# Kernel tuning notes

Measured on AMD Instinct MI355X. Metric: run time of the kernel, lower is better.

Reference implementation:

```python
import jax, jax.numpy as jnp
import numpy as np

B, T, D, H, L = 32, 512, 1024, 1024, 2


def setup_inputs() -> dict:
    key = jax.random.key(0)
    ks = jax.random.split(key, 7)
    s_in = 1.0 / np.sqrt(D)
    s_h = 1.0 / np.sqrt(H)
    return {
        "x": jax.random.normal(ks[0], (B, T, D), dtype=jnp.float32),
        # layer 0: input_size = D
        "W_ih0": jax.random.uniform(ks[1], (4 * H, D), jnp.float32, -s_in, s_in),
        "b0": jax.random.uniform(ks[2], (4 * H,), jnp.float32, -s_in, s_in),
        "W_hh0": jax.random.uniform(ks[3], (4 * H, H), jnp.float32, -s_h, s_h),
        # layer 1: input_size = H
        "W_ih1": jax.random.uniform(ks[4], (4 * H, H), jnp.float32, -s_h, s_h),
        "b1": jax.random.uniform(ks[5], (4 * H,), jnp.float32, -s_h, s_h),
        "W_hh1": jax.random.uniform(ks[6], (4 * H, H), jnp.float32, -s_h, s_h),
    }


def _lstm_layer(x_seq, W_ih, b, W_hh):
    # x_seq: [T, B, Din]. Precompute the input-to-gate GEMM for all steps
    # (mathematically identical to per-step, but one big GEMM).
    gx = jnp.einsum('tbd,gd->tbg', x_seq, W_ih) + b  # [T, B, 4H]
    h0 = jnp.zeros((x_seq.shape[1], W_hh.shape[1]), x_seq.dtype)
    c0 = jnp.zeros_like(h0)

    def step(carry, gx_t):
        h, c = carry
        gates = gx_t + h @ W_hh.T  # [B, 4H]
        i, f, g, o = jnp.split(gates, 4, axis=-1)  # torch chunk order: i,f,g,o
        i = jax.nn.sigmoid(i)
        f = jax.nn.sigmoid(f)
        g = jnp.tanh(g)
        o = jax.nn.sigmoid(o)
        c_new = f * c + i * g
        h_new = o * jnp.tanh(c_new)
        return (h_new, c_new), h_new

    (h_n, c_n), hs = jax.lax.scan(step, (h0, c0), gx)
    return hs, h_n, c_n  # hs: [T, B, H]


def reference(x, W_ih0, b0, W_hh0, W_ih1, b1, W_hh1):
    xs = jnp.transpose(x, (1, 0, 2))  # batch_first -> [T, B, D]
    hs0, h0_n, c0_n = _lstm_layer(xs, W_ih0, b0, W_hh0)
    hs1, h1_n, c1_n = _lstm_layer(hs0, W_ih1, b1, W_hh1)
    output = jnp.transpose(hs1, (1, 0, 2))  # [B, T, H]
    h_n = jnp.stack([h0_n, h1_n], axis=0)  # [L, B, H]
    c_n = jnp.stack([c0_n, c1_n], axis=0)
    return output, (h_n, c_n)
```

## Files before the change

kernel.cpp:

```cpp
#include <hip/hip_runtime.h>
#include <stdint.h>

typedef __attribute__((ext_vector_type(8))) short short8;
typedef __attribute__((ext_vector_type(4))) short short4v;
typedef __attribute__((ext_vector_type(4))) float f32x4;
typedef __attribute__((ext_vector_type(4))) unsigned int u32x4;
typedef __attribute__((ext_vector_type(4))) int i32x4;
typedef __attribute__((ext_vector_type(2))) unsigned long long u64x2;

__device__ inline unsigned short f2bf(float f) {
  unsigned int u = __builtin_bit_cast(unsigned int, f);
  u += 0x7fffu + ((u >> 16) & 1u);
  return (unsigned short)(u >> 16);
}
__device__ inline float bf2f(unsigned short s) {
  return __builtin_bit_cast(float, (unsigned int)s << 16);
}

__device__ inline unsigned long long stale64(unsigned long long v) {
  unsigned long long x = v ^ 0x7f7f7f7f7f7f7f7full;
  return (x - 0x0001000100010001ull) & ~x & 0x8000800080008000ull;
}


__global__ __launch_bounds__(256) void cvt_w_kernel(const float* __restrict__ W,
                                                    short* __restrict__ Wp) {
  const int total = (4096 * 1024) / 4;
  for (int i = blockIdx.x * blockDim.x + threadIdx.x; i < total;
       i += gridDim.x * blockDim.x) {
    int k4 = i & 255;
    int n  = i >> 8;
    int g = n & 3, j = n >> 2;
    float4 v = *(const float4*)(W + ((size_t)g * 1024 + j) * 1024 + (size_t)k4 * 4);
    short4v o;
    o.x = (short)f2bf(v.x); o.y = (short)f2bf(v.y);
    o.z = (short)f2bf(v.z); o.w = (short)f2bf(v.w);
    *(short4v*)(Wp + (size_t)n * 1024 + k4 * 4) = o;
  }
}

__global__ __launch_bounds__(256) void cvt_b_kernel(const float* __restrict__ b,
                                                    float* __restrict__ bp) {
  int n = blockIdx.x * blockDim.x + threadIdx.x;
  if (n < 4096) bp[n] = b[(n & 3) * 1024 + (n >> 2)];
}

__global__ __launch_bounds__(256) void gemm_btx(const short* __restrict__ A,
                                                const float* __restrict__ x,
                                                short* __restrict__ C) {
  const int n0 = blockIdx.x * 128;
  const int m0 = blockIdx.y * 128;
  const int tid = threadIdx.x;
  const int lane = tid & 63, wid = tid >> 6;
  const int wr = wid >> 1, wc = wid & 1;
  const int fr = lane & 15, fq = lane >> 4;

  __shared__ __align__(16) short As[128 * 32];
  __shared__ __align__(16) short Bs[128 * 32];

  f32x4 acc[4][4];
#pragma unroll
  for (int i = 0; i < 4; i++)
#pragma unroll
    for (int j = 0; j < 4; j++) acc[i][j] = (f32x4){0.f, 0.f, 0.f, 0.f};

  for (int kt = 0; kt < 1024; kt += 32) {
#pragma unroll
    for (int s = 0; s < 2; s++) {
      int c = tid + s * 256;
      int row = c >> 2;
      int off = (c & 3) * 8;
      *(u32x4*)&As[row * 32 + off] =
          *(const u32x4*)(A + (size_t)(n0 + row) * 1024 + kt + off);
      int m = m0 + row;
      int tt = m >> 5, bb = m & 31;
      const float* xp = x + ((size_t)bb * 512 + tt) * 1024 + kt + off;
      float4 va = *(const float4*)xp;
      float4 vb = *(const float4*)(xp + 4);
      short8 o;
      o[0] = (short)f2bf(va.x); o[1] = (short)f2bf(va.y);
      o[2] = (short)f2bf(va.z); o[3] = (short)f2bf(va.w);
      o[4] = (short)f2bf(vb.x); o[5] = (short)f2bf(vb.y);
      o[6] = (short)f2bf(vb.z); o[7] = (short)f2bf(vb.w);
      *(short8*)&Bs[row * 32 + off] = o;
    }
    __syncthreads();
    short8 af[4], bf[4];
#pragma unroll
    for (int i = 0; i < 4; i++)
      af[i] = *(const short8*)&As[(wr * 64 + i * 16 + fr) * 32 + fq * 8];
#pragma unroll
    for (int j = 0; j < 4; j++)
      bf[j] = *(const short8*)&Bs[(wc * 64 + j * 16 + fr) * 32 + fq * 8];
#pragma unroll
    for (int i = 0; i < 4; i++)
#pragma unroll
      for (int j = 0; j < 4; j++)
        acc[i][j] = __builtin_amdgcn_mfma_f32_16x16x32_bf16(af[i], bf[j], acc[i][j], 0, 0, 0);
    __syncthreads();
  }

#pragma unroll
  for (int i = 0; i < 4; i++) {
#pragma unroll
    for (int j = 0; j < 4; j++) {
      int nq = n0 + wr * 64 + i * 16 + fq * 4;
      int m = m0 + wc * 64 + j * 16 + fr;
      int t = m >> 5, b = m & 31;
      unsigned long long pk = 0;
#pragma unroll
      for (int r = 0; r < 4; r++)
        pk |= (unsigned long long)f2bf(acc[i][j][r]) << (16 * r);
      *(unsigned long long*)&C[(size_t)t * 131072 + (size_t)b * 4096 + nq] = pk;
    }
  }
}

#define POLL8(HBP)                                                            \
  do {                                                                        \
    i32x4 r0, r1, r2, r3, r4, r5, r6, r7;                                     \
    while (true) {                                                            \
      asm volatile(                                                           \
          "global_load_dwordx4 %0, %8, %16 sc0 sc1\n\t"                       \
          "global_load_dwordx4 %1, %9, %16 sc0 sc1\n\t"                       \
          "global_load_dwordx4 %2, %10, %16 sc0 sc1\n\t"                      \
          "global_load_dwordx4 %3, %11, %16 sc0 sc1\n\t"                      \
          "global_load_dwordx4 %4, %12, %16 sc0 sc1\n\t"                      \
          "global_load_dwordx4 %5, %13, %16 sc0 sc1\n\t"                      \
          "global_load_dwordx4 %6, %14, %16 sc0 sc1\n\t"                      \
          "global_load_dwordx4 %7, %15, %16 sc0 sc1\n\t"                      \
          "s_waitcnt vmcnt(0)"                                                \
          : "=&v"(r0), "=&v"(r1), "=&v"(r2), "=&v"(r3), "=&v"(r4),            \
            "=&v"(r5), "=&v"(r6), "=&v"(r7)                                   \
          : "v"(soff[0]), "v"(soff[1]), "v"(soff[2]), "v"(soff[3]),           \
            "v"(soff[4]), "v"(soff[5]), "v"(soff[6]), "v"(soff[7]),           \
            "s"(HBP)                                                          \
          : "memory");                                                        \
      u64x2 q0 = __builtin_bit_cast(u64x2, r0), q1 = __builtin_bit_cast(u64x2, r1); \
      u64x2 q2 = __builtin_bit_cast(u64x2, r2), q3 = __builtin_bit_cast(u64x2, r3); \
      u64x2 q4 = __builtin_bit_cast(u64x2, r4), q5 = __builtin_bit_cast(u64x2, r5); \
      u64x2 q6 = __builtin_bit_cast(u64x2, r6), q7 = __builtin_bit_cast(u64x2, r7); \
      unsigned long long bad =                                                \
          stale64(q0.x) | stale64(q0.y) | stale64(q1.x) | stale64(q1.y) |     \
          stale64(q2.x) | stale64(q2.y) | stale64(q3.x) | stale64(q3.y) |     \
          stale64(q4.x) | stale64(q4.y) | stale64(q5.x) | stale64(q5.y) |     \
          stale64(q6.x) | stale64(q6.y) | stale64(q7.x) | stale64(q7.y);      \
      if (!bad) break;                                                        \
    }                                                                         \
    *(i32x4*)&img[widx[0]] = r0;                                              \
    *(i32x4*)&img[widx[1]] = r1;                                              \
    *(i32x4*)&img[widx[2]] = r2;                                              \
    *(i32x4*)&img[widx[3]] = r3;                                              \
    *(i32x4*)&img[widx[4]] = r4;                                              \
    *(i32x4*)&img[widx[5]] = r5;                                              \
    *(i32x4*)&img[widx[6]] = r6;                                              \
    *(i32x4*)&img[widx[7]] = r7;                                              \
  } while (0)

__global__ __launch_bounds__(512, 1) void lstm_fused(
    const short* __restrict__ gx0, const short* __restrict__ whh0,
    const float* __restrict__ b0p, const short* __restrict__ wih1,
    const short* __restrict__ whh1, const float* __restrict__ b1p,
    short* __restrict__ hs0, short* __restrict__ hs1,
    float* __restrict__ out, float* __restrict__ hn, float* __restrict__ cn) {
  const int tid = threadIdx.x;
  const int lane = tid & 63, w = tid >> 6;
  const int fr = lane & 15, fq = lane >> 4;

  __shared__ __align__(16) short img[32 * 1024];
  __shared__ __align__(16) float red[4 * 64 * 4];

  if (blockIdx.x < 64) {
    const int rg = (int)blockIdx.x >> 1, bg = (int)blockIdx.x & 1;
    const int n_base = rg * 128 + w * 16;
    const int b = bg * 16 + fr;
    const int jb = rg * 32 + w * 4;
    const int j = jb + fq;
    const int sw = fr & 7;

    const short* arow = whh0 + (size_t)(n_base + fr) * 1024 + fq * 8;
    short8 wreg[32];
#pragma unroll
    for (int kk = 0; kk < 32; kk++) wreg[kk] = *(const short8*)(arow + kk * 32);

    float bia[4];
#pragma unroll
    for (int r = 0; r < 4; r++) bia[r] = b0p[n_base + fq * 4 + r];

    unsigned int soff[4];
    int widx[4];
#pragma unroll
    for (int i = 0; i < 4; i++) {
      int ch = tid + i * 512;
      soff[i] = (unsigned int)ch * 16;
      int bb = ch >> 7, cc = ch & 127;
      widx[i] = bb * 1024 + ((cc ^ (bb & 7)) << 3);
    }

    float cell = 0.f;
    for (int t = 0; t < 512; ++t) {
      unsigned long long gq = *(const unsigned long long*)(
          gx0 + (size_t)t * 131072 + (size_t)b * 4096 + n_base + fq * 4);

      if (t > 0) {
        const short* hbp = hs0 + (size_t)(t - 1) * 32768 + bg * 16384;
        i32x4 r0, r1, r2, r3;
        while (true) {
          asm volatile(
              "global_load_dwordx4 %0, %4, %8 sc0 sc1\n\t"
              "global_load_dwordx4 %1, %5, %8 sc0 sc1\n\t"
              "global_load_dwordx4 %2, %6, %8 sc0 sc1\n\t"
              "global_load_dwordx4 %3, %7, %8 sc0 sc1\n\t"
              "s_waitcnt vmcnt(0)"
              : "=&v"(r0), "=&v"(r1), "=&v"(r2), "=&v"(r3)
              : "v"(soff[0]), "v"(soff[1]), "v"(soff[2]), "v"(soff[3]),
                "s"(hbp)
              : "memory");
          u64x2 q0 = __builtin_bit_cast(u64x2, r0);
          u64x2 q1 = __builtin_bit_cast(u64x2, r1);
          u64x2 q2 = __builtin_bit_cast(u64x2, r2);
          u64x2 q3 = __builtin_bit_cast(u64x2, r3);
          unsigned long long bad =
              stale64(q0.x) | stale64(q0.y) | stale64(q1.x) | stale64(q1.y) |
              stale64(q2.x) | stale64(q2.y) | stale64(q3.x) | stale64(q3.y);
          if (!bad) break;
        }
        *(i32x4*)&img[widx[0]] = r0;
        *(i32x4*)&img[widx[1]] = r1;
        *(i32x4*)&img[widx[2]] = r2;
        *(i32x4*)&img[widx[3]] = r3;
      }
      __syncthreads();

      f32x4 a0 = (f32x4){0.f,0.f,0.f,0.f}, a1 = (f32x4){0.f,0.f,0.f,0.f};
      f32x4 a2 = (f32x4){0.f,0.f,0.f,0.f}, a3 = (f32x4){0.f,0.f,0.f,0.f};
      if (t > 0) {
#pragma unroll
        for (int m = 0; m < 8; m++) {
          const int chb = fq + m * 16;
          short8 bv0 = *(const short8*)&img[fr * 1024 + (((chb + 0) ^ sw) << 3)];
          short8 bv1 = *(const short8*)&img[fr * 1024 + (((chb + 4) ^ sw) << 3)];
          short8 bv2 = *(const short8*)&img[fr * 1024 + (((chb + 8) ^ sw) << 3)];
          short8 bv3 = *(const short8*)&img[fr * 1024 + (((chb + 12) ^ sw) << 3)];
          a0 = __builtin_amdgcn_mfma_f32_16x16x32_bf16(wreg[4 * m + 0], bv0, a0, 0, 0, 0);
          a1 = __builtin_amdgcn_mfma_f32_16x16x32_bf16(wreg[4 * m + 1], bv1, a1, 0, 0, 0);
          a2 = __builtin_amdgcn_mfma_f32_16x16x32_bf16(wreg[4 * m + 2], bv2, a2, 0, 0, 0);
          a3 = __builtin_amdgcn_mfma_f32_16x16x32_bf16(wreg[4 * m + 3], bv3, a3, 0, 0, 0);
        }
      }

      float pre0 = (a0[0] + a1[0]) + (a2[0] + a3[0]) + bf2f((unsigned short)(gq & 0xFFFF)) + bia[0];
      float pre1 = (a0[1] + a1[1]) + (a2[1] + a3[1]) + bf2f((unsigned short)((gq >> 16) & 0xFFFF)) + bia[1];
      float pre2 = (a0[2] + a1[2]) + (a2[2] + a3[2]) + bf2f((unsigned short)((gq >> 32) & 0xFFFF)) + bia[2];
      float pre3 = (a0[3] + a1[3]) + (a2[3] + a3[3]) + bf2f((unsigned short)((gq >> 48) & 0xFFFF)) + bia[3];

      float iv = 1.f / (1.f + __expf(-pre0));
      float fv = 1.f / (1.f + __expf(-pre1));
      float gv = 2.f / (1.f + __expf(-2.f * pre2)) - 1.f;
      float ov = 1.f / (1.f + __expf(-pre3));
      cell = fv * cell + iv * gv;
      float h = ov * (2.f / (1.f + __expf(-2.f * cell)) - 1.f);

      unsigned int hu = (unsigned int)f2bf(h);
      unsigned int v1 = __shfl(hu, fr + 16);
      unsigned int v2 = __shfl(hu, fr + 32);
      unsigned int v3 = __shfl(hu, fr + 48);
      if (fq == 0) {
        unsigned long long pk = (unsigned long long)hu |
                                ((unsigned long long)v1 << 16) |
                                ((unsigned long long)v2 << 32) |
                                ((unsigned long long)v3 << 48);
        __hip_atomic_store(
            (unsigned long long*)(hs0 + (size_t)t * 32768 + (size_t)b * 1024 + jb),
            pk, __ATOMIC_RELAXED, __HIP_MEMORY_SCOPE_AGENT);
      }
      if (t == 511) {
        hn[b * 1024 + j] = h;
        cn[b * 1024 + j] = cell;
        break;
      }
      __syncthreads();
    }
  } else {
    const int idx = (int)blockIdx.x - 64;
    const int rg = idx >> 1, bg = idx & 1;
    const int wn = w & 3, mw = w >> 2;
    const int n_base = rg * 64 + wn * 16;
    const int b = bg * 16 + fr;
    const int jb = rg * 16 + wn * 4;
    const int j = jb + fq;
    const int sw = fr & 7;
    const int ib = mw << 14;

    const short* wsrc = mw ? wih1 : whh1;
    const short* arow = wsrc + (size_t)(n_base + fr) * 1024 + fq * 8;
    short8 wreg[32];
#pragma unroll
    for (int kk = 0; kk < 32; kk++) wreg[kk] = *(const short8*)(arow + kk * 32);

    float bia[4];
#pragma unroll
    for (int r = 0; r < 4; r++) bia[r] = b1p[n_base + fq * 4 + r];

    const int lt = tid & 255;
    unsigned int soff[8];
    int widx[8];
#pragma unroll
    for (int i = 0; i < 8; i++) {
      int ch = lt + i * 256;
      soff[i] = (unsigned int)ch * 16;
      int bb = ch >> 7, cc = ch & 127;
      widx[i] = ib + bb * 1024 + ((cc ^ (bb & 7)) << 3);
    }

    float cell = 0.f;
    for (int t = 0; t < 512; ++t) {
      if (mw) {
        const short* hbp = hs0 + (size_t)t * 32768 + bg * 16384;
        POLL8(hbp);
      } else if (t > 0) {
        const short* hbp = hs1 + (size_t)(t - 1) * 32768 + bg * 16384;
        POLL8(hbp);
      }
      __syncthreads();

      f32x4 a0 = (f32x4){0.f,0.f,0.f,0.f}, a1 = (f32x4){0.f,0.f,0.f,0.f};
      f32x4 a2 = (f32x4){0.f,0.f,0.f,0.f}, a3 = (f32x4){0.f,0.f,0.f,0.f};
      if (mw || t > 0) {
#pragma unroll
        for (int m = 0; m < 8; m++) {
          const int chb = fq + m * 16;
          short8 bv0 = *(const short8*)&img[ib + fr * 1024 + (((chb + 0) ^ sw) << 3)];
          short8 bv1 = *(const short8*)&img[ib + fr * 1024 + (((chb + 4) ^ sw) << 3)];
          short8 bv2 = *(const short8*)&img[ib + fr * 1024 + (((chb + 8) ^ sw) << 3)];
          short8 bv3 = *(const short8*)&img[ib + fr * 1024 + (((chb + 12) ^ sw) << 3)];
          a0 = __builtin_amdgcn_mfma_f32_16x16x32_bf16(wreg[4 * m + 0], bv0, a0, 0, 0, 0);
          a1 = __builtin_amdgcn_mfma_f32_16x16x32_bf16(wreg[4 * m + 1], bv1, a1, 0, 0, 0);
          a2 = __builtin_amdgcn_mfma_f32_16x16x32_bf16(wreg[4 * m + 2], bv2, a2, 0, 0, 0);
          a3 = __builtin_amdgcn_mfma_f32_16x16x32_bf16(wreg[4 * m + 3], bv3, a3, 0, 0, 0);
        }
      }
      f32x4 s4 = (a0 + a1) + (a2 + a3);
      if (mw) *(f32x4*)&red[(wn * 64 + lane) * 4] = s4;
      __syncthreads();

      if (!mw) {
        const f32x4 o4 = *(const f32x4*)&red[(wn * 64 + lane) * 4];
        float pre0 = s4[0] + o4[0] + bia[0];
        float pre1 = s4[1] + o4[1] + bia[1];
        float pre2 = s4[2] + o4[2] + bia[2];
        float pre3 = s4[3] + o4[3] + bia[3];

        float iv = 1.f / (1.f + __expf(-pre0));
        float fv = 1.f / (1.f + __expf(-pre1));
        float gv = 2.f / (1.f + __expf(-2.f * pre2)) - 1.f;
        float ov = 1.f / (1.f + __expf(-pre3));
        cell = fv * cell + iv * gv;
        float h = ov * (2.f / (1.f + __expf(-2.f * cell)) - 1.f);

        unsigned int hu = (unsigned int)f2bf(h);
        unsigned int v1 = __shfl(hu, fr + 16);
        unsigned int v2 = __shfl(hu, fr + 32);
        unsigned int v3 = __shfl(hu, fr + 48);
        if (fq == 0) {
          unsigned long long pk = (unsigned long long)hu |
                                  ((unsigned long long)v1 << 16) |
                                  ((unsigned long long)v2 << 32) |
                                  ((unsigned long long)v3 << 48);
          __hip_atomic_store(
              (unsigned long long*)(hs1 + (size_t)t * 32768 + (size_t)b * 1024 + jb),
              pk, __ATOMIC_RELAXED, __HIP_MEMORY_SCOPE_AGENT);
        }
        out[(size_t)b * 524288 + (size_t)t * 1024 + j] = h;
        if (t == 511) {
          hn[32768 + b * 1024 + j] = h;
          cn[32768 + b * 1024 + j] = cell;
        }
      }
      if (t == 511) break;
      __syncthreads();
    }
  }
}

extern "C" void kernel_launch(void* const* d_in, const int* in_sizes, int n_in,
                              void* d_out, int out_size, void* d_ws, size_t ws_size,
                              hipStream_t stream) {
  const float* x    = (const float*)d_in[0];
  const float* Wih0 = (const float*)d_in[1];
  const float* b0   = (const float*)d_in[2];
  const float* Whh0 = (const float*)d_in[3];
  const float* Wih1 = (const float*)d_in[4];
  const float* b1   = (const float*)d_in[5];
  const float* Whh1 = (const float*)d_in[6];

  float* out = (float*)d_out;
  float* hn  = out + 16777216;
  float* cn  = hn + 65536;

  char* ws = (char*)d_ws;
  size_t off = 0;
  auto carve = [&](size_t bytes) {
    char* p = ws + off;
    off += (bytes + 255) & ~(size_t)255;
    return p;
  };
  short* wih0p = (short*)carve(4096ull * 1024 * 2);
  short* whh0p = (short*)carve(4096ull * 1024 * 2);
  short* wih1p = (short*)carve(4096ull * 1024 * 2);
  short* whh1p = (short*)carve(4096ull * 1024 * 2);
  float* b0p   = (float*)carve(4096 * 4);
  float* b1p   = (float*)carve(4096 * 4);
  short* gx    = (short*)carve(512ull * 4096 * 32 * 2);
  short* hs0   = (short*)carve(16384ull * 1024 * 2);
  short* hs1   = (short*)carve(16384ull * 1024 * 2);

  hipLaunchKernelGGL(cvt_w_kernel, dim3(1024), dim3(256), 0, stream, Wih0, wih0p);
  hipLaunchKernelGGL(cvt_w_kernel, dim3(1024), dim3(256), 0, stream, Whh0, whh0p);
  hipLaunchKernelGGL(cvt_w_kernel, dim3(1024), dim3(256), 0, stream, Wih1, wih1p);
  hipLaunchKernelGGL(cvt_w_kernel, dim3(1024), dim3(256), 0, stream, Whh1, whh1p);
  hipLaunchKernelGGL(cvt_b_kernel, dim3(16), dim3(256), 0, stream, b0, b0p);
  hipLaunchKernelGGL(cvt_b_kernel, dim3(16), dim3(256), 0, stream, b1, b1p);
  (void)hipMemsetAsync(hs0, 0x7F, 16384ull * 1024 * 2, stream);
  (void)hipMemsetAsync(hs1, 0x7F, 16384ull * 1024 * 2, stream);

  hipLaunchKernelGGL(gemm_btx, dim3(32, 128), dim3(256), 0, stream,
                     (const short*)wih0p, x, gx);

  hipLaunchKernelGGL(lstm_fused, dim3(192), dim3(512), 0, stream,
                     (const short*)gx, (const short*)whh0p, (const float*)b0p,
                     (const short*)wih1p, (const short*)whh1p, (const float*)b1p,
                     hs0, hs1, out, hn, cn);
}
```

Baseline: 2.096 ms.

## Software-pipeline layer-1 input projection one step ahead of recurrence

```diff
diff --git a/kernel.cpp b/kernel.cpp
--- a/kernel.cpp
+++ b/kernel.cpp
@@ -157,6 +157,25 @@
     *(i32x4*)&img[widx[7]] = r7;                                              \
   } while (0)
 
+#define L1_MFMA(S4)                                                           \
+  {                                                                           \
+    f32x4 a0_ = (f32x4){0.f,0.f,0.f,0.f}, a1_ = (f32x4){0.f,0.f,0.f,0.f};     \
+    f32x4 a2_ = (f32x4){0.f,0.f,0.f,0.f}, a3_ = (f32x4){0.f,0.f,0.f,0.f};     \
+    _Pragma("unroll")                                                         \
+    for (int m = 0; m < 8; m++) {                                             \
+      const int chb = fq + m * 16;                                            \
+      short8 bv0 = *(const short8*)&img[ib + fr * 1024 + (((chb + 0) ^ sw) << 3)]; \
+      short8 bv1 = *(const short8*)&img[ib + fr * 1024 + (((chb + 4) ^ sw) << 3)]; \
+      short8 bv2 = *(const short8*)&img[ib + fr * 1024 + (((chb + 8) ^ sw) << 3)]; \
+      short8 bv3 = *(const short8*)&img[ib + fr * 1024 + (((chb + 12) ^ sw) << 3)]; \
+      a0_ = __builtin_amdgcn_mfma_f32_16x16x32_bf16(wreg[4 * m + 0], bv0, a0_, 0, 0, 0); \
+      a1_ = __builtin_amdgcn_mfma_f32_16x16x32_bf16(wreg[4 * m + 1], bv1, a1_, 0, 0, 0); \
+      a2_ = __builtin_amdgcn_mfma_f32_16x16x32_bf16(wreg[4 * m + 2], bv2, a2_, 0, 0, 0); \
+      a3_ = __builtin_amdgcn_mfma_f32_16x16x32_bf16(wreg[4 * m + 3], bv3, a3_, 0, 0, 0); \
+    }                                                                         \
+    S4 = (a0_ + a1_) + (a2_ + a3_);                                           \
+  }
+
 __global__ __launch_bounds__(512, 1) void lstm_fused(
     const short* __restrict__ gx0, const short* __restrict__ whh0,
     const float* __restrict__ b0p, const short* __restrict__ wih1,
@@ -168,7 +187,7 @@
   const int fr = lane & 15, fq = lane >> 4;
 
   __shared__ __align__(16) short img[32 * 1024];
-  __shared__ __align__(16) float red[4 * 64 * 4];
+  __shared__ __align__(16) float red[2][1024];
 
   if (blockIdx.x < 64) {
     const int rg = (int)blockIdx.x >> 1, bg = (int)blockIdx.x & 1;
@@ -313,39 +332,41 @@
       widx[i] = ib + bb * 1024 + ((cc ^ (bb & 7)) << 3);
     }
 
+    if (mw) {
+      const short* hbp = hs0 + bg * 16384;
+      POLL8(hbp);
+    }
+    __syncthreads();
+    if (mw) {
+      f32x4 s4;
+      L1_MFMA(s4);
+      *(f32x4*)&red[0][(wn * 64 + lane) * 4] = s4;
+    }
+    __syncthreads();
+
     float cell = 0.f;
     for (int t = 0; t < 512; ++t) {
       if (mw) {
-        const short* hbp = hs0 + (size_t)t * 32768 + bg * 16384;
-        POLL8(hbp);
+        if (t < 511) {
+          const short* hbp = hs0 + (size_t)(t + 1) * 32768 + bg * 16384;
+          POLL8(hbp);
+        }
       } else if (t > 0) {
         const short* hbp = hs1 + (size_t)(t - 1) * 32768 + bg * 16384;
         POLL8(hbp);
       }
       __syncthreads();
 
-      f32x4 a0 = (f32x4){0.f,0.f,0.f,0.f}, a1 = (f32x4){0.f,0.f,0.f,0.f};
-      f32x4 a2 = (f32x4){0.f,0.f,0.f,0.f}, a3 = (f32x4){0.f,0.f,0.f,0.f};
-      if (mw || t > 0) {
-#pragma unroll
-        for (int m = 0; m < 8; m++) {
-          const int chb = fq + m * 16;
-          short8 bv0 = *(const short8*)&img[ib + fr * 1024 + (((chb + 0) ^ sw) << 3)];
-          short8 bv1 = *(const short8*)&img[ib + fr * 1024 + (((chb + 4) ^ sw) << 3)];
-          short8 bv2 = *(const short8*)&img[ib + fr * 1024 + (((chb + 8) ^ sw) << 3)];
-          short8 bv3 = *(const short8*)&img[ib + fr * 1024 + (((chb + 12) ^ sw) << 3)];
-          a0 = __builtin_amdgcn_mfma_f32_16x16x32_bf16(wreg[4 * m + 0], bv0, a0, 0, 0, 0);
-          a1 = __builtin_amdgcn_mfma_f32_16x16x32_bf16(wreg[4 * m + 1], bv1, a1, 0, 0, 0);
-          a2 = __builtin_amdgcn_mfma_f32_16x16x32_bf16(wreg[4 * m + 2], bv2, a2, 0, 0, 0);
-          a3 = __builtin_amdgcn_mfma_f32_16x16x32_bf16(wreg[4 * m + 3], bv3, a3, 0, 0, 0);
-        }
-      }
-      f32x4 s4 = (a0 + a1) + (a2 + a3);
-      if (mw) *(f32x4*)&red[(wn * 64 + lane) * 4] = s4;
-      __syncthreads();
-
-      if (!mw) {
-        const f32x4 o4 = *(const f32x4*)&red[(wn * 64 + lane) * 4];
+      if (mw) {
+        if (t < 511) {
+          f32x4 s4;
+          L1_MFMA(s4);
+          *(f32x4*)&red[(t + 1) & 1][(wn * 64 + lane) * 4] = s4;
+        }
+      } else {
+        f32x4 s4 = (f32x4){0.f, 0.f, 0.f, 0.f};
+        if (t > 0) L1_MFMA(s4);
+        const f32x4 o4 = *(const f32x4*)&red[t & 1][(wn * 64 + lane) * 4];
         float pre0 = s4[0] + o4[0] + bia[0];
         float pre1 = s4[1] + o4[1] + bia[1];
         float pre2 = s4[2] + o4[2] + bia[2];
```

After: 2.367 ms. 1.13x slower.
